# Performance work log

Measured on AMD Instinct MI355X. Metric: run time of the kernel, lower is better.

Reference implementation:

```python
import jax, jax.numpy as jnp
import numpy as np

BETA = 0.25
NUM_VECTORS = 1024
LATENT_DIM = 256

def setup_inputs() -> dict:
    key = jax.random.key(0)
    k1, k2 = jax.random.split(key)
    z = jax.random.normal(k1, (32, LATENT_DIM, 64, 64), dtype=jnp.float32)
    # embedding initialized uniform(-1/K, 1/K) as in the torch module
    emb = jax.random.uniform(k2, (NUM_VECTORS, LATENT_DIM), dtype=jnp.float32,
                             minval=-1.0 / NUM_VECTORS, maxval=1.0 / NUM_VECTORS)
    return {"z": z, "emb": emb}

def reference(z, emb):
    B, C, H, W = z.shape
    zp = jnp.transpose(z, (0, 2, 3, 1))            # [B,H,W,C]
    zf = zp.reshape(-1, C)                          # [N,C]
    # pairwise squared L2 distances: ||z||^2 + ||e||^2 - 2 z e^T -> [N,K]
    d = (jnp.sum(zf * zf, axis=-1, keepdims=True)
         + jnp.sum(emb * emb, axis=-1)
         - 2.0 * (zf @ emb.T))
    idx = jnp.argmin(d, axis=1)                     # [N]
    zq = emb[idx].reshape(B, H, W, C)               # gather + reshape
    # loss exactly as source: mse(zq, sg(z)) - beta * mse(z, sg(zq))
    loss = (jnp.mean((zq - jax.lax.stop_gradient(zp)) ** 2)
            - BETA * jnp.mean((zp - jax.lax.stop_gradient(zq)) ** 2))
    # straight-through estimator
    zq_st = zp + jax.lax.stop_gradient(zq - zp)
    zq_out = jnp.transpose(zq_st, (0, 3, 1, 2))     # back to [B,C,H,W]
    return zq_out, idx, loss
```

## Files before the change

### kernel.cpp

```cpp
#include <hip/hip_runtime.h>
#include <stdint.h>

#define B_   32
#define C_   256
#define HW_  4096
#define N_   131072
#define K_   1024

typedef __attribute__((ext_vector_type(8))) short bf16x8;
typedef __attribute__((ext_vector_type(4))) float f32x4;

__device__ __forceinline__ unsigned short f2bf(float f) {
    unsigned int x = __float_as_uint(f);
    return (unsigned short)((x + 0x7FFFu + ((x >> 16) & 1u)) >> 16);
}
__device__ __forceinline__ float bf2f(unsigned short h) {
    return __uint_as_float(((unsigned int)h) << 16);
}

#define GLD16(g, l) __builtin_amdgcn_global_load_lds((const __attribute__((address_space(1))) void*)(g), \
                        (__attribute__((address_space(3))) void*)(l), 16, 0, 0)

__global__ void ee_kernel(const float* __restrict__ emb, float* __restrict__ ee) {
#pragma clang fp contract(off)
    int k = blockIdx.x * blockDim.x + threadIdx.x;
    if (k >= K_) return;
    const float* e = emb + (size_t)k * C_;
    float res = 0.f;
    for (int h = 0; h < 2; ++h) {
        float r[8];
        #pragma unroll
        for (int j = 0; j < 8; ++j) { float v = e[h*128 + j]; r[j] = v * v; }
        for (int i = 8; i < 128; i += 8) {
            #pragma unroll
            for (int j = 0; j < 8; ++j) { float v = e[h*128 + i + j]; r[j] += v * v; }
        }
        float s = ((r[0] + r[1]) + (r[2] + r[3])) + ((r[4] + r[5]) + (r[6] + r[7]));
        res += s;
    }
    ee[k] = res;
}

__global__ void esplit_kernel(const float* __restrict__ emb,
                              unsigned short* __restrict__ eh, unsigned short* __restrict__ el) {
    int t = blockIdx.x * 256 + threadIdx.x;
    int k = t >> 5, c8 = (t & 31) * 8;
    const float* src = emb + (size_t)k * C_ + c8;
    unsigned short hb[8], lb[8];
    #pragma unroll
    for (int i = 0; i < 8; ++i) {
        float f = src[i];
        unsigned short h = f2bf(f);
        hb[i] = h; lb[i] = f2bf(f - bf2f(h));
    }
    size_t off = (size_t)k * C_ + c8;
    *(uint4*)&eh[off] = *(uint4*)hb;
    *(uint4*)&el[off] = *(uint4*)lb;
}

__global__ void zsplit_kernel(const float* __restrict__ z,
                              unsigned short* __restrict__ zh, unsigned short* __restrict__ zl) {
    __shared__ float t[64][65];
    int blk = blockIdx.x;
    int b = blk >> 8, ct = (blk >> 6) & 3, ht = blk & 63;
    int tid = threadIdx.x;
    int hw = tid & 63, c0 = tid >> 6;
    const float* src = z + ((size_t)b * C_ + ct * 64) * HW_ + ht * 64;
    #pragma unroll
    for (int k = 0; k < 16; ++k) {
        int c = k * 4 + c0;
        t[c][hw] = src[(size_t)c * HW_ + hw];
    }
    __syncthreads();
    int hw2 = tid >> 2, cs = (tid & 3) * 16;
    size_t off = ((size_t)b * HW_ + ht * 64 + hw2) * C_ + ct * 64 + cs;
    unsigned short hb[16], lb[16];
    #pragma unroll
    for (int i = 0; i < 16; ++i) {
        float f = t[cs + i][hw2];
        unsigned short h = f2bf(f);
        hb[i] = h; lb[i] = f2bf(f - bf2f(h));
    }
    *(uint4*)&zh[off]     = *(uint4*)&hb[0];
    *(uint4*)&zh[off + 8] = *(uint4*)&hb[8];
    *(uint4*)&zl[off]     = *(uint4*)&lb[0];
    *(uint4*)&zl[off + 8] = *(uint4*)&lb[8];
}

#define INS3(T, P) do { uint32_t _p = (P); \
    if (_p < T[2]) { if (_p < T[1]) { T[2] = T[1]; \
        if (_p < T[0]) { T[1] = T[0]; T[0] = _p; } else T[1] = _p; } else T[2] = _p; } } while (0)

__launch_bounds__(256)
__global__ void mfma_argmin_kernel(const unsigned short* __restrict__ zh, const unsigned short* __restrict__ zl,
                                   const unsigned short* __restrict__ eh, const unsigned short* __restrict__ el,
                                   const float* __restrict__ ee, uint32_t* __restrict__ top3) {
    __shared__ unsigned short Ah[128*32], Al[128*32], Bh[128*32], Bl[128*32];
    __shared__ float eesh[K_];
    __shared__ uint32_t red[128][2][3];

    const int tid = threadIdx.x;
    const int lane = tid & 63, wave = tid >> 6;
    const int wr = wave >> 1, wc = wave & 1;
    const int row0 = blockIdx.x * 128;

    for (int i = tid; i < K_; i += 256) eesh[i] = ee[i];

    uint32_t t3[16][3];
    #pragma unroll
    for (int s = 0; s < 16; ++s) { t3[s][0] = 0xFFFFFFFFu; t3[s][1] = 0xFFFFFFFFu; t3[s][2] = 0xFFFFFFFFu; }

    const int lr  = lane >> 2;
    const int lc8 = (((lane & 3) ^ ((lr >> 1) & 3)) * 8);
    const int fr  = lane & 15;
    const int fk  = (((lane >> 4) ^ ((fr >> 1) & 3)) * 8);
    const int rb  = wave * 32;

    __syncthreads();

    for (int kt = 0; kt < 8; ++kt) {
        f32x4 acc[4][4];
        #pragma unroll
        for (int m = 0; m < 4; ++m)
            #pragma unroll
            for (int n = 0; n < 4; ++n) acc[m][n] = (f32x4){0.f, 0.f, 0.f, 0.f};

        for (int c0 = 0; c0 < C_; c0 += 32) {
            size_t ga0 = (size_t)(row0 + rb + lr) * C_ + c0 + lc8;
            size_t ga1 = ga0 + (size_t)16 * C_;
            size_t gb0 = (size_t)(kt * 128 + rb + lr) * C_ + c0 + lc8;
            size_t gb1 = gb0 + (size_t)16 * C_;
            GLD16(zh + ga0, &Ah[(rb +  0) * 32]);
            GLD16(zh + ga1, &Ah[(rb + 16) * 32]);
            GLD16(zl + ga0, &Al[(rb +  0) * 32]);
            GLD16(zl + ga1, &Al[(rb + 16) * 32]);
            GLD16(eh + gb0, &Bh[(rb +  0) * 32]);
            GLD16(eh + gb1, &Bh[(rb + 16) * 32]);
            GLD16(el + gb0, &Bl[(rb +  0) * 32]);
            GLD16(el + gb1, &Bl[(rb + 16) * 32]);
            __syncthreads();

            bf16x8 ah[4], al4[4], bh[4], bl4[4];
            #pragma unroll
            for (int m = 0; m < 4; ++m) {
                int r = wr * 64 + m * 16 + fr;
                ah[m]  = *(const bf16x8*)&Ah[r * 32 + fk];
                al4[m] = *(const bf16x8*)&Al[r * 32 + fk];
            }
            #pragma unroll
            for (int n = 0; n < 4; ++n) {
                int r = wc * 64 + n * 16 + fr;
                bh[n]  = *(const bf16x8*)&Bh[r * 32 + fk];
                bl4[n] = *(const bf16x8*)&Bl[r * 32 + fk];
            }
            #pragma unroll
            for (int m = 0; m < 4; ++m)
                #pragma unroll
                for (int n = 0; n < 4; ++n) {
                    acc[m][n] = __builtin_amdgcn_mfma_f32_16x16x32_bf16(ah[m],  bh[n],  acc[m][n], 0, 0, 0);
                    acc[m][n] = __builtin_amdgcn_mfma_f32_16x16x32_bf16(ah[m],  bl4[n], acc[m][n], 0, 0, 0);
                    acc[m][n] = __builtin_amdgcn_mfma_f32_16x16x32_bf16(al4[m], bh[n],  acc[m][n], 0, 0, 0);
                }
            __syncthreads();
        }

        #pragma unroll
        for (int n = 0; n < 4; ++n) {
            int col = kt * 128 + wc * 64 + n * 16 + fr;
            float eev = eesh[col];
            #pragma unroll
            for (int m = 0; m < 4; ++m) {
                #pragma unroll
                for (int j = 0; j < 4; ++j) {
                    float d = eev - 2.0f * acc[m][n][j];
                    uint32_t bbits = __float_as_uint(d);
                    uint32_t u = bbits ^ (0x80000000u | (uint32_t)((int32_t)bbits >> 31));
                    uint32_t p = (u & 0xFFFFFC00u) | (uint32_t)col;
                    INS3(t3[m * 4 + j], p);
                }
            }
        }
    }

    #pragma unroll
    for (int st = 1; st < 16; st <<= 1) {
        #pragma unroll
        for (int s = 0; s < 16; ++s) {
            uint32_t q0 = __shfl_xor(t3[s][0], st, 64);
            uint32_t q1 = __shfl_xor(t3[s][1], st, 64);
            uint32_t q2 = __shfl_xor(t3[s][2], st, 64);
            INS3(t3[s], q0); INS3(t3[s], q1); INS3(t3[s], q2);
        }
    }
    if ((lane & 15) == 0) {
        int g = lane >> 4;
        #pragma unroll
        for (int m = 0; m < 4; ++m)
            #pragma unroll
            for (int j = 0; j < 4; ++j) {
                int r = wr * 64 + m * 16 + g * 4 + j;
                int s = m * 4 + j;
                red[r][wc][0] = t3[s][0]; red[r][wc][1] = t3[s][1]; red[r][wc][2] = t3[s][2];
            }
    }
    __syncthreads();
    if (tid < 128) {
        uint32_t a0 = red[tid][0][0], a1 = red[tid][0][1], a2 = red[tid][0][2];
        uint32_t b0 = red[tid][1][0], b1 = red[tid][1][1], b2 = red[tid][1][2];
        uint32_t o0, o1, o2;
        if (a0 <= b0) { o0 = a0;
            if (a1 <= b0) { o1 = a1; o2 = (a2 < b0 ? a2 : b0); }
            else          { o1 = b0; o2 = (a1 < b1 ? a1 : b1); }
        } else { o0 = b0;
            if (b1 <= a0) { o1 = b1; o2 = (b2 < a0 ? b2 : a0); }
            else          { o1 = a0; o2 = (a1 < b1 ? a1 : b1); }
        }
        uint32_t* dst = top3 + (size_t)(row0 + tid) * 3;
        dst[0] = o0; dst[1] = o1; dst[2] = o2;
    }
}

__launch_bounds__(256)
__global__ void refine_kernel(const float* __restrict__ z, const float* __restrict__ emb,
                              const float* __restrict__ ee, const uint32_t* __restrict__ top3,
                              int* __restrict__ idx_i, float* __restrict__ idx_f) {
#pragma clang fp contract(off)
    int n = blockIdx.x * 256 + threadIdx.x;
    int b = n >> 12, hw = n & 4095;
    int c0 = (int)(top3[(size_t)n * 3 + 0] & 0x3FFu);
    int c1 = (int)(top3[(size_t)n * 3 + 1] & 0x3FFu);
    int c2 = (int)(top3[(size_t)n * 3 + 2] & 0x3FFu);
    int t;
    if (c1 < c0) { t = c0; c0 = c1; c1 = t; }
    if (c2 < c1) { t = c1; c1 = c2; c2 = t; }
    if (c1 < c0) { t = c0; c0 = c1; c1 = t; }
    const float* zp = z + (size_t)b * C_ * HW_ + hw;
    const float4* e0 = (const float4*)(emb + (size_t)c0 * C_);
    const float4* e1 = (const float4*)(emb + (size_t)c1 * C_);
    const float4* e2 = (const float4*)(emb + (size_t)c2 * C_);
    float a0 = 0.f, a1 = 0.f, a2 = 0.f;
    float zzr = 0.f;

    #pragma unroll
    for (int half = 0; half < 2; ++half) {
        float r[8];
        #pragma unroll 2
        for (int c4l = 0; c4l < 2; ++c4l) {
            int c4 = half * 32 + c4l;
            float4 v0 = e0[c4], v1 = e1[c4], v2 = e2[c4];
            #pragma unroll
            for (int i = 0; i < 4; ++i) {
                int c = c4 * 4 + i;
                float zv = zp[(size_t)c * HW_];
                r[c4l * 4 + i] = zv * zv;
                a0 = fmaf(zv, ((const float*)&v0)[i], a0);
                a1 = fmaf(zv, ((const float*)&v1)[i], a1);
                a2 = fmaf(zv, ((const float*)&v2)[i], a2);
            }
        }
        #pragma unroll 6
        for (int c4l = 2; c4l < 32; ++c4l) {
            int c4 = half * 32 + c4l;
            float4 v0 = e0[c4], v1 = e1[c4], v2 = e2[c4];
            #pragma unroll
            for (int i = 0; i < 4; ++i) {
                int c = c4 * 4 + i;
                float zv = zp[(size_t)c * HW_];
                float sq = zv * zv;
                int j = (c4l * 4 + i) & 7;
                r[j] = r[j] + sq;
                a0 = fmaf(zv, ((const float*)&v0)[i], a0);
                a1 = fmaf(zv, ((const float*)&v1)[i], a1);
                a2 = fmaf(zv, ((const float*)&v2)[i], a2);
            }
        }
        float s = ((r[0] + r[1]) + (r[2] + r[3])) + ((r[4] + r[5]) + (r[6] + r[7]));
        zzr = zzr + s;
    }

    float A0 = zzr + ee[c0]; float d0 = A0 - 2.0f * a0;
    float A1 = zzr + ee[c1]; float d1 = A1 - 2.0f * a1;
    float A2 = zzr + ee[c2]; float d2 = A2 - 2.0f * a2;
    float bv = d0; int bi = c0;
    if (c1 != c0 && d1 < bv) { bv = d1; bi = c1; }
    if (c2 != c1 && c2 != c0 && d2 < bv) { bv = d2; bi = c2; }
    idx_i[n] = bi;
    idx_f[n] = (float)bi;
}

__global__ void gather_kernel(const float* __restrict__ z, const float* __restrict__ emb,
                              const int* __restrict__ idx, float* __restrict__ zq,
                              float* __restrict__ partials) {
#pragma clang fp contract(off)
    const long long TOT = (long long)N_ * (C_/4);
    float ls = 0.f;
    for (long long g = (long long)blockIdx.x * blockDim.x + threadIdx.x; g < TOT;
         g += (long long)gridDim.x * blockDim.x) {
        int c4 = (int)(g >> 17);
        int n  = (int)(g & (N_ - 1));
        int b = n >> 12, hw = n & 4095;
        int j = idx[n];
        float4 e4 = *(const float4*)&emb[(size_t)j * C_ + c4*4];
        size_t base = (size_t)b * C_ * HW_ + (size_t)(c4*4) * HW_ + hw;
        float zv, df;
        zv = z[base + 0*HW_]; df = e4.x - zv; zq[base + 0*HW_] = zv + df; ls += df*df;
        zv = z[base + 1*HW_]; df = e4.y - zv; zq[base + 1*HW_] = zv + df; ls += df*df;
        zv = z[base + 2*HW_]; df = e4.z - zv; zq[base + 2*HW_] = zv + df; ls += df*df;
        zv = z[base + 3*HW_]; df = e4.w - zv; zq[base + 3*HW_] = zv + df; ls += df*df;
    }
    __shared__ float sred[256];
    sred[threadIdx.x] = ls;
    __syncthreads();
    for (int s = 128; s > 0; s >>= 1) {
        if (threadIdx.x < s) sred[threadIdx.x] += sred[threadIdx.x + s];
        __syncthreads();
    }
    if (threadIdx.x == 0) partials[blockIdx.x] = sred[0];
}

__global__ void finalize_kernel(const float* __restrict__ partials, int nparts,
                                float* __restrict__ loss_out) {
    __shared__ float sred[256];
    float s = 0.f;
    for (int i = threadIdx.x; i < nparts; i += 256) s += partials[i];
    sred[threadIdx.x] = s; __syncthreads();
    for (int st = 128; st > 0; st >>= 1) {
        if (threadIdx.x < st) sred[threadIdx.x] += sred[threadIdx.x + st];
        __syncthreads();
    }
    if (threadIdx.x == 0) {
        float m = sred[0] / 33554432.0f;
        *loss_out = m - 0.25f * m;
    }
}

extern "C" void kernel_launch(void* const* d_in, const int* in_sizes, int n_in,
                              void* d_out, int out_size, void* d_ws, size_t ws_size,
                              hipStream_t stream) {
    const float* z   = (const float*)d_in[0];
    const float* emb = (const float*)d_in[1];
    float* out   = (float*)d_out;
    float* zq    = out;
    float* idx_f = out + (size_t)N_ * C_;
    float* loss  = idx_f + N_;

    unsigned short* zh = (unsigned short*)d_out;
    unsigned short* zl = zh + (size_t)N_ * C_;

    float*     ee       = (float*)d_ws;
    int*       idx_i    = (int*)(ee + K_);
    uint32_t*  top3     = (uint32_t*)(idx_i + N_);
    float*     partials = (float*)(top3 + (size_t)3 * N_);
    unsigned short* eh  = (unsigned short*)(partials + 2048);
    unsigned short* el  = eh + (size_t)K_ * C_;

    esplit_kernel<<<128, 256, 0, stream>>>(emb, eh, el);
    ee_kernel<<<(K_ + 255)/256, 256, 0, stream>>>(emb, ee);
    zsplit_kernel<<<8192, 256, 0, stream>>>(z, zh, zl);
    mfma_argmin_kernel<<<N_/128, 256, 0, stream>>>(zh, zl, eh, el, ee, top3);
    refine_kernel<<<N_/256, 256, 0, stream>>>(z, emb, ee, top3, idx_i, idx_f);
    gather_kernel<<<2048, 256, 0, stream>>>(z, emb, idx_i, zq, partials);
    finalize_kernel<<<1, 256, 0, stream>>>(partials, 2048, loss);
}
```

Measured before the change: 719.3 us.

## Double-buffer MFMA argmin, keep top-2 candidates, refine only ambiguous rows

The MFMA argmin kernel now double-buffers its LDS tiles across a flattened 64-step loop, so the next tile's loads are issued before the current tile's MFMAs and one barrier per step is removed. It keeps a top-2 list of full-precision 64-bit packed distances instead of a top-3 list with truncated distances. A triage kernel accepts rows whose top-2 gap exceeds a threshold and queues only the remaining rows for exact fp32 recomputation, which replaces the full-N refine pass. This relies on the threshold being safe given the error of the bf16 hi/lo split, trades a third candidate for a gap test, and adds an atomic counter plus an extra launch. The needy list reuses the el buffer area, and el is still read by the argmin kernel that runs before the list is written.

```diff
diff --git a/kernel.cpp b/kernel.cpp
--- a/kernel.cpp
+++ b/kernel.cpp
@@ -6,9 +6,11 @@
 #define HW_  4096
 #define N_   131072
 #define K_   1024
+#define GAP_THR 1.25e-4f
 
 typedef __attribute__((ext_vector_type(8))) short bf16x8;
 typedef __attribute__((ext_vector_type(4))) float f32x4;
+typedef unsigned long long u64;
 
 __device__ __forceinline__ unsigned short f2bf(float f) {
     unsigned int x = __float_as_uint(f);
@@ -16,6 +18,16 @@
 }
 __device__ __forceinline__ float bf2f(unsigned short h) {
     return __uint_as_float(((unsigned int)h) << 16);
+}
+__device__ __forceinline__ u64 shfl_xor64(u64 v, int m) {
+    int lo = __shfl_xor((int)(v & 0xFFFFFFFFull), m, 64);
+    int hi = __shfl_xor((int)(v >> 32), m, 64);
+    return ((u64)(unsigned int)hi << 32) | (unsigned int)lo;
+}
+__device__ __forceinline__ float unpack_d(u64 p) {
+    uint32_t u = (uint32_t)(p >> 10);
+    uint32_t b = (u & 0x80000000u) ? (u ^ 0x80000000u) : ~u;
+    return __uint_as_float(b);
 }
 
 #define GLD16(g, l) __builtin_amdgcn_global_load_lds((const __attribute__((address_space(1))) void*)(g), \
@@ -87,17 +99,16 @@
     *(uint4*)&zl[off + 8] = *(uint4*)&lb[8];
 }
 
-#define INS3(T, P) do { uint32_t _p = (P); \
-    if (_p < T[2]) { if (_p < T[1]) { T[2] = T[1]; \
-        if (_p < T[0]) { T[1] = T[0]; T[0] = _p; } else T[1] = _p; } else T[2] = _p; } } while (0)
+#define INS2(T0, T1, P) do { u64 _p = (P); \
+    if (_p < T1) { if (_p < T0) { T1 = T0; T0 = _p; } else T1 = _p; } } while (0)
 
 __launch_bounds__(256)
 __global__ void mfma_argmin_kernel(const unsigned short* __restrict__ zh, const unsigned short* __restrict__ zl,
                                    const unsigned short* __restrict__ eh, const unsigned short* __restrict__ el,
-                                   const float* __restrict__ ee, uint32_t* __restrict__ top3) {
-    __shared__ unsigned short Ah[128*32], Al[128*32], Bh[128*32], Bl[128*32];
+                                   const float* __restrict__ ee, ulonglong2* __restrict__ top2) {
+    __shared__ unsigned short Ah[2][128*32], Al[2][128*32], Bh[2][128*32], Bl[2][128*32];
     __shared__ float eesh[K_];
-    __shared__ uint32_t red[128][2][3];
+    __shared__ u64 red[128][2][2];
 
     const int tid = threadIdx.x;
     const int lane = tid & 63, wave = tid >> 6;
@@ -106,9 +117,9 @@
 
     for (int i = tid; i < K_; i += 256) eesh[i] = ee[i];
 
-    uint32_t t3[16][3];
-    #pragma unroll
-    for (int s = 0; s < 16; ++s) { t3[s][0] = 0xFFFFFFFFu; t3[s][1] = 0xFFFFFFFFu; t3[s][2] = 0xFFFFFFFFu; }
+    u64 t0[16], t1[16];
+    #pragma unroll
+    for (int s = 0; s < 16; ++s) { t0[s] = ~0ull; t1[s] = ~0ull; }
 
     const int lr  = lane >> 2;
     const int lc8 = (((lane & 3) ^ ((lr >> 1) & 3)) * 8);
@@ -116,80 +127,90 @@
     const int fk  = (((lane >> 4) ^ ((fr >> 1) & 3)) * 8);
     const int rb  = wave * 32;
 
+#define STAGE(bf, step) do { int _kt = (step) >> 3, _c0 = ((step) & 7) * 32;            \
+        size_t ga0 = (size_t)(row0 + rb + lr) * C_ + _c0 + lc8;                         \
+        size_t ga1 = ga0 + (size_t)16 * C_;                                             \
+        size_t gb0 = (size_t)(_kt * 128 + rb + lr) * C_ + _c0 + lc8;                    \
+        size_t gb1 = gb0 + (size_t)16 * C_;                                             \
+        GLD16(zh + ga0, &Ah[bf][(rb +  0) * 32]);                                       \
+        GLD16(zh + ga1, &Ah[bf][(rb + 16) * 32]);                                       \
+        GLD16(zl + ga0, &Al[bf][(rb +  0) * 32]);                                       \
+        GLD16(zl + ga1, &Al[bf][(rb + 16) * 32]);                                       \
+        GLD16(eh + gb0, &Bh[bf][(rb +  0) * 32]);                                       \
+        GLD16(eh + gb1, &Bh[bf][(rb + 16) * 32]);                                       \
+        GLD16(el + gb0, &Bl[bf][(rb +  0) * 32]);                                       \
+        GLD16(el + gb1, &Bl[bf][(rb + 16) * 32]);                                       \
+    } while (0)
+
+    f32x4 acc[4][4];
+    #pragma unroll
+    for (int m = 0; m < 4; ++m)
+        #pragma unroll
+        for (int n = 0; n < 4; ++n) acc[m][n] = (f32x4){0.f, 0.f, 0.f, 0.f};
+
+    STAGE(0, 0);
     __syncthreads();
 
-    for (int kt = 0; kt < 8; ++kt) {
-        f32x4 acc[4][4];
+    for (int s = 0; s < 64; ++s) {
+        if (s < 63) STAGE((s + 1) & 1, s + 1);
+        const int bf = s & 1;
+
+        bf16x8 ah[4], al4[4], bh[4], bl4[4];
+        #pragma unroll
+        for (int m = 0; m < 4; ++m) {
+            int r = wr * 64 + m * 16 + fr;
+            ah[m]  = *(const bf16x8*)&Ah[bf][r * 32 + fk];
+            al4[m] = *(const bf16x8*)&Al[bf][r * 32 + fk];
+        }
+        #pragma unroll
+        for (int n = 0; n < 4; ++n) {
+            int r = wc * 64 + n * 16 + fr;
+            bh[n]  = *(const bf16x8*)&Bh[bf][r * 32 + fk];
+            bl4[n] = *(const bf16x8*)&Bl[bf][r * 32 + fk];
+        }
         #pragma unroll
         for (int m = 0; m < 4; ++m)
             #pragma unroll
-            for (int n = 0; n < 4; ++n) acc[m][n] = (f32x4){0.f, 0.f, 0.f, 0.f};
-
-        for (int c0 = 0; c0 < C_; c0 += 32) {
-            size_t ga0 = (size_t)(row0 + rb + lr) * C_ + c0 + lc8;
-            size_t ga1 = ga0 + (size_t)16 * C_;
-            size_t gb0 = (size_t)(kt * 128 + rb + lr) * C_ + c0 + lc8;
-            size_t gb1 = gb0 + (size_t)16 * C_;
-            GLD16(zh + ga0, &Ah[(rb +  0) * 32]);
-            GLD16(zh + ga1, &Ah[(rb + 16) * 32]);
-            GLD16(zl + ga0, &Al[(rb +  0) * 32]);
-            GLD16(zl + ga1, &Al[(rb + 16) * 32]);
-            GLD16(eh + gb0, &Bh[(rb +  0) * 32]);
-            GLD16(eh + gb1, &Bh[(rb + 16) * 32]);
-            GLD16(el + gb0, &Bl[(rb +  0) * 32]);
-            GLD16(el + gb1, &Bl[(rb + 16) * 32]);
-            __syncthreads();
-
-            bf16x8 ah[4], al4[4], bh[4], bl4[4];
-            #pragma unroll
-            for (int m = 0; m < 4; ++m) {
-                int r = wr * 64 + m * 16 + fr;
-                ah[m]  = *(const bf16x8*)&Ah[r * 32 + fk];
-                al4[m] = *(const bf16x8*)&Al[r * 32 + fk];
-            }
-            #pragma unroll
             for (int n = 0; n < 4; ++n) {
-                int r = wc * 64 + n * 16 + fr;
-                bh[n]  = *(const bf16x8*)&Bh[r * 32 + fk];
-                bl4[n] = *(const bf16x8*)&Bl[r * 32 + fk];
+                acc[m][n] = __builtin_amdgcn_mfma_f32_16x16x32_bf16(ah[m],  bh[n],  acc[m][n], 0, 0, 0);
+                acc[m][n] = __builtin_amdgcn_mfma_f32_16x16x32_bf16(ah[m],  bl4[n], acc[m][n], 0, 0, 0);
+                acc[m][n] = __builtin_amdgcn_mfma_f32_16x16x32_bf16(al4[m], bh[n],  acc[m][n], 0, 0, 0);
+            }
+
+        if ((s & 7) == 7) {
+            int kt = s >> 3;
+            #pragma unroll
+            for (int n = 0; n < 4; ++n) {
+                int col = kt * 128 + wc * 64 + n * 16 + fr;
+                float eev = eesh[col];
+                #pragma unroll
+                for (int m = 0; m < 4; ++m) {
+                    #pragma unroll
+                    for (int j = 0; j < 4; ++j) {
+                        float d = eev - 2.0f * acc[m][n][j];
+                        uint32_t bb = __float_as_uint(d);
+                        uint32_t u = bb ^ (0x80000000u | (uint32_t)((int32_t)bb >> 31));
+                        u64 p = ((u64)u << 10) | (uint32_t)col;
+                        int sl = m * 4 + j;
+                        INS2(t0[sl], t1[sl], p);
+                    }
+                }
             }
             #pragma unroll
             for (int m = 0; m < 4; ++m)
                 #pragma unroll
-                for (int n = 0; n < 4; ++n) {
-                    acc[m][n] = __builtin_amdgcn_mfma_f32_16x16x32_bf16(ah[m],  bh[n],  acc[m][n], 0, 0, 0);
-                    acc[m][n] = __builtin_amdgcn_mfma_f32_16x16x32_bf16(ah[m],  bl4[n], acc[m][n], 0, 0, 0);
-                    acc[m][n] = __builtin_amdgcn_mfma_f32_16x16x32_bf16(al4[m], bh[n],  acc[m][n], 0, 0, 0);
-                }
-            __syncthreads();
-        }
-
-        #pragma unroll
-        for (int n = 0; n < 4; ++n) {
-            int col = kt * 128 + wc * 64 + n * 16 + fr;
-            float eev = eesh[col];
-            #pragma unroll
-            for (int m = 0; m < 4; ++m) {
-                #pragma unroll
-                for (int j = 0; j < 4; ++j) {
-                    float d = eev - 2.0f * acc[m][n][j];
-                    uint32_t bbits = __float_as_uint(d);
-                    uint32_t u = bbits ^ (0x80000000u | (uint32_t)((int32_t)bbits >> 31));
-                    uint32_t p = (u & 0xFFFFFC00u) | (uint32_t)col;
-                    INS3(t3[m * 4 + j], p);
-                }
-            }
-        }
+                for (int n = 0; n < 4; ++n) acc[m][n] = (f32x4){0.f, 0.f, 0.f, 0.f};
+        }
+        __syncthreads();
     }
 
     #pragma unroll
     for (int st = 1; st < 16; st <<= 1) {
         #pragma unroll
         for (int s = 0; s < 16; ++s) {
-            uint32_t q0 = __shfl_xor(t3[s][0], st, 64);
-            uint32_t q1 = __shfl_xor(t3[s][1], st, 64);
-            uint32_t q2 = __shfl_xor(t3[s][2], st, 64);
-            INS3(t3[s], q0); INS3(t3[s], q1); INS3(t3[s], q2);
+            u64 q0 = shfl_xor64(t0[s], st);
+            u64 q1 = shfl_xor64(t1[s], st);
+            INS2(t0[s], t1[s], q0); INS2(t0[s], t1[s], q1);
         }
     }
     if ((lane & 15) == 0) {
@@ -199,93 +220,97 @@
             #pragma unroll
             for (int j = 0; j < 4; ++j) {
                 int r = wr * 64 + m * 16 + g * 4 + j;
-                int s = m * 4 + j;
-                red[r][wc][0] = t3[s][0]; red[r][wc][1] = t3[s][1]; red[r][wc][2] = t3[s][2];
+                int sl = m * 4 + j;
+                red[r][wc][0] = t0[sl]; red[r][wc][1] = t1[sl];
             }
     }
     __syncthreads();
     if (tid < 128) {
-        uint32_t a0 = red[tid][0][0], a1 = red[tid][0][1], a2 = red[tid][0][2];
-        uint32_t b0 = red[tid][1][0], b1 = red[tid][1][1], b2 = red[tid][1][2];
-        uint32_t o0, o1, o2;
-        if (a0 <= b0) { o0 = a0;
-            if (a1 <= b0) { o1 = a1; o2 = (a2 < b0 ? a2 : b0); }
-            else          { o1 = b0; o2 = (a1 < b1 ? a1 : b1); }
-        } else { o0 = b0;
-            if (b1 <= a0) { o1 = b1; o2 = (b2 < a0 ? b2 : a0); }
-            else          { o1 = a0; o2 = (a1 < b1 ? a1 : b1); }
-        }
-        uint32_t* dst = top3 + (size_t)(row0 + tid) * 3;
-        dst[0] = o0; dst[1] = o1; dst[2] = o2;
+        u64 a0 = red[tid][0][0], a1 = red[tid][0][1];
+        u64 b0 = red[tid][1][0], b1 = red[tid][1][1];
+        u64 o0, o1;
+        if (a0 <= b0) { o0 = a0; o1 = (a1 < b0 ? a1 : b0); }
+        else          { o0 = b0; o1 = (b1 < a0 ? b1 : a0); }
+        top2[row0 + tid] = make_ulonglong2(o0, o1);
+    }
+#undef STAGE
+}
+
+__global__ void triage_kernel(const ulonglong2* __restrict__ top2,
+                              int* __restrict__ idx_i, float* __restrict__ idx_f,
+                              uint32_t* __restrict__ counter, uint32_t* __restrict__ needy) {
+    int n = blockIdx.x * 256 + threadIdx.x;
+    ulonglong2 t = top2[n];
+    float d0 = unpack_d(t.x), d1 = unpack_d(t.y);
+    if (d1 - d0 > GAP_THR) {
+        int i0 = (int)(t.x & 0x3FFull);
+        idx_i[n] = i0; idx_f[n] = (float)i0;
+    } else {
+        uint32_t p = atomicAdd(counter, 1u);
+        needy[p] = (uint32_t)n;
     }
 }
 
 __launch_bounds__(256)
-__global__ void refine_kernel(const float* __restrict__ z, const float* __restrict__ emb,
-                              const float* __restrict__ ee, const uint32_t* __restrict__ top3,
+__global__ void exact2_kernel(const float* __restrict__ z, const float* __restrict__ emb,
+                              const float* __restrict__ ee, const ulonglong2* __restrict__ top2,
+                              const uint32_t* __restrict__ counter, const uint32_t* __restrict__ needy,
                               int* __restrict__ idx_i, float* __restrict__ idx_f) {
 #pragma clang fp contract(off)
-    int n = blockIdx.x * 256 + threadIdx.x;
-    int b = n >> 12, hw = n & 4095;
-    int c0 = (int)(top3[(size_t)n * 3 + 0] & 0x3FFu);
-    int c1 = (int)(top3[(size_t)n * 3 + 1] & 0x3FFu);
-    int c2 = (int)(top3[(size_t)n * 3 + 2] & 0x3FFu);
-    int t;
-    if (c1 < c0) { t = c0; c0 = c1; c1 = t; }
-    if (c2 < c1) { t = c1; c1 = c2; c2 = t; }
-    if (c1 < c0) { t = c0; c0 = c1; c1 = t; }
-    const float* zp = z + (size_t)b * C_ * HW_ + hw;
-    const float4* e0 = (const float4*)(emb + (size_t)c0 * C_);
-    const float4* e1 = (const float4*)(emb + (size_t)c1 * C_);
-    const float4* e2 = (const float4*)(emb + (size_t)c2 * C_);
-    float a0 = 0.f, a1 = 0.f, a2 = 0.f;
-    float zzr = 0.f;
-
-    #pragma unroll
-    for (int half = 0; half < 2; ++half) {
-        float r[8];
-        #pragma unroll 2
-        for (int c4l = 0; c4l < 2; ++c4l) {
-            int c4 = half * 32 + c4l;
-            float4 v0 = e0[c4], v1 = e1[c4], v2 = e2[c4];
-            #pragma unroll
-            for (int i = 0; i < 4; ++i) {
-                int c = c4 * 4 + i;
-                float zv = zp[(size_t)c * HW_];
-                r[c4l * 4 + i] = zv * zv;
-                a0 = fmaf(zv, ((const float*)&v0)[i], a0);
-                a1 = fmaf(zv, ((const float*)&v1)[i], a1);
-                a2 = fmaf(zv, ((const float*)&v2)[i], a2);
-            }
-        }
-        #pragma unroll 6
-        for (int c4l = 2; c4l < 32; ++c4l) {
-            int c4 = half * 32 + c4l;
-            float4 v0 = e0[c4], v1 = e1[c4], v2 = e2[c4];
-            #pragma unroll
-            for (int i = 0; i < 4; ++i) {
-                int c = c4 * 4 + i;
-                float zv = zp[(size_t)c * HW_];
-                float sq = zv * zv;
-                int j = (c4l * 4 + i) & 7;
-                r[j] = r[j] + sq;
-                a0 = fmaf(zv, ((const float*)&v0)[i], a0);
-                a1 = fmaf(zv, ((const float*)&v1)[i], a1);
-                a2 = fmaf(zv, ((const float*)&v2)[i], a2);
-            }
-        }
-        float s = ((r[0] + r[1]) + (r[2] + r[3])) + ((r[4] + r[5]) + (r[6] + r[7]));
-        zzr = zzr + s;
-    }
-
-    float A0 = zzr + ee[c0]; float d0 = A0 - 2.0f * a0;
-    float A1 = zzr + ee[c1]; float d1 = A1 - 2.0f * a1;
-    float A2 = zzr + ee[c2]; float d2 = A2 - 2.0f * a2;
-    float bv = d0; int bi = c0;
-    if (c1 != c0 && d1 < bv) { bv = d1; bi = c1; }
-    if (c2 != c1 && c2 != c0 && d2 < bv) { bv = d2; bi = c2; }
-    idx_i[n] = bi;
-    idx_f[n] = (float)bi;
+    uint32_t cnt = *counter;
+    for (uint32_t g = blockIdx.x * 256 + threadIdx.x; g < cnt; g += gridDim.x * 256) {
+        int n = (int)needy[g];
+        int b = n >> 12, hw = n & 4095;
+        ulonglong2 tt = top2[n];
+        int c0 = (int)(tt.x & 0x3FFull);
+        int c1 = (int)(tt.y & 0x3FFull);
+        if (c1 < c0) { int t = c0; c0 = c1; c1 = t; }
+        const float* zp = z + (size_t)b * C_ * HW_ + hw;
+        const float4* e0 = (const float4*)(emb + (size_t)c0 * C_);
+        const float4* e1 = (const float4*)(emb + (size_t)c1 * C_);
+        float a0 = 0.f, a1 = 0.f;
+        float zzr = 0.f;
+        #pragma unroll
+        for (int half = 0; half < 2; ++half) {
+            float r[8];
+            #pragma unroll 2
+            for (int c4l = 0; c4l < 2; ++c4l) {
+                int c4 = half * 32 + c4l;
+                float4 v0 = e0[c4], v1 = e1[c4];
+                #pragma unroll
+                for (int i = 0; i < 4; ++i) {
+                    int c = c4 * 4 + i;
+                    float zv = zp[(size_t)c * HW_];
+                    r[c4l * 4 + i] = zv * zv;
+                    a0 = fmaf(zv, ((const float*)&v0)[i], a0);
+                    a1 = fmaf(zv, ((const float*)&v1)[i], a1);
+                }
+            }
+            #pragma unroll 6
+            for (int c4l = 2; c4l < 32; ++c4l) {
+                int c4 = half * 32 + c4l;
+                float4 v0 = e0[c4], v1 = e1[c4];
+                #pragma unroll
+                for (int i = 0; i < 4; ++i) {
+                    int c = c4 * 4 + i;
+                    float zv = zp[(size_t)c * HW_];
+                    float sq = zv * zv;
+                    int j = (c4l * 4 + i) & 7;
+                    r[j] = r[j] + sq;
+                    a0 = fmaf(zv, ((const float*)&v0)[i], a0);
+                    a1 = fmaf(zv, ((const float*)&v1)[i], a1);
+                }
+            }
+            float s = ((r[0] + r[1]) + (r[2] + r[3])) + ((r[4] + r[5]) + (r[6] + r[7]));
+            zzr = zzr + s;
+        }
+        float A0 = zzr + ee[c0]; float d0 = A0 - 2.0f * a0;
+        float A1 = zzr + ee[c1]; float d1 = A1 - 2.0f * a1;
+        int bi = c0;
+        if (d1 < d0) bi = c1;
+        idx_i[n] = bi;
+        idx_f[n] = (float)bi;
+    }
 }
 
 __global__ void gather_kernel(const float* __restrict__ z, const float* __restrict__ emb,
@@ -347,18 +372,22 @@
     unsigned short* zh = (unsigned short*)d_out;
     unsigned short* zl = zh + (size_t)N_ * C_;
 
-    float*     ee       = (float*)d_ws;
-    int*       idx_i    = (int*)(ee + K_);
-    uint32_t*  top3     = (uint32_t*)(idx_i + N_);
-    float*     partials = (float*)(top3 + (size_t)3 * N_);
-    unsigned short* eh  = (unsigned short*)(partials + 2048);
-    unsigned short* el  = eh + (size_t)K_ * C_;
-
+    float*      ee       = (float*)d_ws;
+    int*        idx_i    = (int*)(ee + K_);
+    ulonglong2* top2     = (ulonglong2*)(idx_i + N_);
+    float*      partials = (float*)(top2 + N_);
+    uint32_t*   counter  = (uint32_t*)(partials + 2048);
+    unsigned short* eh   = (unsigned short*)(counter + 4);
+    unsigned short* el   = eh + (size_t)K_ * C_;
+    uint32_t*   needy    = (uint32_t*)el;
+
+    hipMemsetAsync(counter, 0, 4, stream);
     esplit_kernel<<<128, 256, 0, stream>>>(emb, eh, el);
     ee_kernel<<<(K_ + 255)/256, 256, 0, stream>>>(emb, ee);
     zsplit_kernel<<<8192, 256, 0, stream>>>(z, zh, zl);
-    mfma_argmin_kernel<<<N_/128, 256, 0, stream>>>(zh, zl, eh, el, ee, top3);
-    refine_kernel<<<N_/256, 256, 0, stream>>>(z, emb, ee, top3, idx_i, idx_f);
+    mfma_argmin_kernel<<<N_/128, 256, 0, stream>>>(zh, zl, eh, el, ee, top2);
+    triage_kernel<<<N_/256, 256, 0, stream>>>(top2, idx_i, idx_f, counter, needy);
+    exact2_kernel<<<64, 256, 0, stream>>>(z, emb, ee, top2, counter, needy, idx_i, idx_f);
     gather_kernel<<<2048, 256, 0, stream>>>(z, emb, idx_i, zq, partials);
     finalize_kernel<<<1, 256, 0, stream>>>(partials, 2048, loss);
 }
```

New measurement: 1.555 ms. 116% more time.
